# Kernel optimization log

Hardware: AMD Instinct MI355X
Metric: run time of the kernel (lower is better)

Reference implementation:

```python
import jax, jax.numpy as jnp
import numpy as np

RADIUS = 0.2
NSAMPLE = 32
USE_XYZ = True
NORMALIZE_XYZ = False


def setup_inputs() -> dict:
    key = jax.random.key(0)
    k1, k2, k3 = jax.random.split(key, 3)
    B, N, S, C = 4, 8192, 2048, 64
    xyz = jax.random.uniform(k1, (B, N, 3), dtype=jnp.float32)
    new_xyz = jax.random.uniform(k2, (B, S, 3), dtype=jnp.float32)
    features = jax.random.normal(k3, (B, C, N), dtype=jnp.float32)
    return {"xyz": xyz, "new_xyz": new_xyz, "features": features}


def _ball_query(new_xyz, xyz, radius, nsample):
    # squared distances [B, S, N] via ||q||^2 + ||p||^2 - 2 q.p (no [B,S,N,3] blowup)
    q2 = jnp.sum(new_xyz * new_xyz, axis=-1)  # [B, S]
    p2 = jnp.sum(xyz * xyz, axis=-1)          # [B, N]
    qp = jnp.einsum('bsd,bnd->bsn', new_xyz, xyz)
    d2 = q2[:, :, None] + p2[:, None, :] - 2.0 * qp
    N = xyz.shape[1]
    in_ball = d2 < radius * radius
    # CUDA ball_query semantics: first nsample indices (in original point order)
    # inside the ball; unfilled slots replicate the first found index.
    scores = jnp.where(in_ball, jnp.arange(N, dtype=jnp.int32), jnp.int32(N))
    sorted_idx = -jax.lax.top_k(-scores, nsample)[0]  # ascending smallest scores
    first = sorted_idx[..., :1]
    idx = jnp.where(sorted_idx < N, sorted_idx, first)
    idx = jnp.where(first < N, idx, 0)  # no neighbors at all -> index 0
    return idx  # [B, S, nsample] int32


def _group(features, idx):
    # features [B, C, N], idx [B, S, K] -> [B, C, S, K]
    return jax.vmap(lambda f, i: f[:, i])(features, idx)


def reference(xyz, new_xyz, features):
    idx = _ball_query(new_xyz, xyz, RADIUS, NSAMPLE)
    xyz_t = jnp.transpose(xyz, (0, 2, 1))  # [B, 3, N]
    grouped_xyz = _group(xyz_t, idx)  # [B, 3, S, K]
    grouped_xyz = grouped_xyz - jnp.transpose(new_xyz, (0, 2, 1))[..., None]
    if NORMALIZE_XYZ:
        grouped_xyz = grouped_xyz / RADIUS
    grouped_features = _group(features, idx)  # [B, C, S, K]
    if USE_XYZ:
        return jnp.concatenate([grouped_xyz, grouped_features], axis=1)
    return grouped_features
```

## Files before the change

kernel.cpp:

```cpp
#include <hip/hip_runtime.h>
#include <hip/hip_bf16.h>
#include <stdint.h>

#define BB 4
#define NN 8192
#define SS 2048
#define CC 64
#define NS 32

typedef unsigned short ushort8 __attribute__((ext_vector_type(8)));

__device__ __forceinline__ unsigned short f2bf(float f) {
    union { float ff; unsigned int i; } v; v.ff = f;
    unsigned int x = v.i;
    x += 0x7fffu + ((x >> 16) & 1u);
    return (unsigned short)(x >> 16);
}
__device__ __forceinline__ float bf2f(unsigned short u) {
    union { unsigned int i; float f; } v; v.i = ((unsigned int)u) << 16; return v.f;
}

__global__ void stage(const float* __restrict__ xyz,
                      const float* __restrict__ feat,
                      float4* __restrict__ pts,
                      unsigned short* __restrict__ ft) {
#pragma clang fp contract(off)
    const int t = threadIdx.x;
    if (blockIdx.x < 128) {
        int i = blockIdx.x * 256 + t;
        const float* p = xyz + (size_t)i * 3;
        float x = p[0], y = p[1], z = p[2];
        float p2 = x * x;
        p2 += y * y;
        p2 += z * z;
        pts[i] = make_float4(x, y, z, p2);
        return;
    }
    __shared__ float tile[64][65];
    const int blk = blockIdx.x - 128;
    const int b  = blk >> 7;
    const int n0 = (blk & 127) * 64;
    const float* fb = feat + (size_t)b * CC * NN;
    const int nq = t & 15;
    #pragma unroll
    for (int it = 0; it < 4; ++it) {
        int c = it * 16 + (t >> 4);
        float4 v = *(const float4*)(fb + (size_t)c * NN + n0 + nq * 4);
        tile[c][nq * 4 + 0] = v.x;
        tile[c][nq * 4 + 1] = v.y;
        tile[c][nq * 4 + 2] = v.z;
        tile[c][nq * 4 + 3] = v.w;
    }
    __syncthreads();
    unsigned short* fo = ft + ((size_t)b * NN + n0) * CC;
    const int oc = t & 7;
    #pragma unroll
    for (int it = 0; it < 2; ++it) {
        int n = it * 32 + (t >> 3);
        ushort8 w;
        #pragma unroll
        for (int j = 0; j < 8; ++j)
            w[j] = f2bf(tile[oc * 8 + j][n]);
        *(ushort8*)(fo + (size_t)n * CC + oc * 8) = w;
    }
}

__launch_bounds__(256)
__global__ void bq_group(const float* __restrict__ new_xyz,
                         const float4* __restrict__ pts,
                         const unsigned short* __restrict__ ft,
                         float* __restrict__ out) {
#pragma clang fp contract(off)
    __shared__ unsigned long long wmask[2][4];
    __shared__ int sidx[NS];
    __shared__ float sfeat[NS][67];
    const int t    = threadIdx.x;
    const int wave = t >> 6;
    const int lane = t & 63;
    const int blk  = blockIdx.x;
    const int b    = blk >> 11;
    const int s    = blk & (SS - 1);

    const float* q = new_xyz + (size_t)(b * SS + s) * 3;
    const float qx = q[0], qy = q[1], qz = q[2];
    const float4* pb = pts + (size_t)b * NN;

    float q2 = qx * qx;
    q2 += qy * qy;
    q2 += qz * qz;

    const unsigned long long below = (1ull << lane) - 1ull;
    int have = 0;
    float4 p = pb[t];
    #pragma unroll 1
    for (int base = 0; base < NN; base += 256) {
        float4 pn = pb[(base + 256 < NN) ? (base + 256 + t) : t];
        float qp = qx * p.x;
        qp += qy * p.y;
        qp += qz * p.z;
        float t1 = q2 + p.w;
        float d2 = t1 - 2.0f * qp;
        bool in = d2 < 0.04f;
        unsigned long long m = __ballot(in);
        const int buf = (base >> 8) & 1;
        if (lane == 0) wmask[buf][wave] = m;
        __syncthreads();
        unsigned long long m0 = wmask[buf][0], m1 = wmask[buf][1],
                           m2 = wmask[buf][2], m3 = wmask[buf][3];
        int pre = __popcll(m & below);
        if (wave > 0) pre += __popcll(m0);
        if (wave > 1) pre += __popcll(m1);
        if (wave > 2) pre += __popcll(m2);
        int pos = have + pre;
        if (in && pos < NS) sidx[pos] = base + t;
        have += __popcll(m0) + __popcll(m1) + __popcll(m2) + __popcll(m3);
        if (have >= NS) break;
        p = pn;
    }
    __syncthreads();
    if (have < NS) {
        int first = (have == 0) ? 0 : sidx[0];
        if (t < NS && t >= have)
            sidx[t] = (have == 0) ? 0 : first;
    }
    __syncthreads();

    const int k  = t & 31;
    const int oc = t >> 5;
    const int idxk = sidx[k];
    {
        const unsigned short* fr = ft + ((size_t)b * NN + idxk) * CC + oc * 8;
        ushort8 v = *(const ushort8*)fr;
        #pragma unroll
        for (int j = 0; j < 8; ++j)
            sfeat[k][3 + oc * 8 + j] = bf2f(v[j]);
    }
    if (t < 96) {
        const int c = t >> 5;
        float4 p3 = pb[idxk];
        float pc = (c == 0) ? p3.x : (c == 1 ? p3.y : p3.z);
        float qc = (c == 0) ? qx : (c == 1 ? qy : qz);
        sfeat[k][c] = pc - qc;
    }
    __syncthreads();

    const size_t plane = (size_t)SS * NS;
    const size_t ob    = (size_t)b * 67 * plane;
    #pragma unroll
    for (int it = 0; it < 3; ++it) {
        int id = t + it * 256;
        if (id < 67 * 8) {
            int ch = id >> 3;
            int kq = id & 7;
            float4 val = make_float4(sfeat[kq * 4 + 0][ch],
                                     sfeat[kq * 4 + 1][ch],
                                     sfeat[kq * 4 + 2][ch],
                                     sfeat[kq * 4 + 3][ch]);
            *(float4*)(out + ob + (size_t)ch * plane + (size_t)s * NS + kq * 4) = val;
        }
    }
}

extern "C" void kernel_launch(void* const* d_in, const int* in_sizes, int n_in,
                              void* d_out, int out_size, void* d_ws, size_t ws_size,
                              hipStream_t stream) {
    const float* xyz     = (const float*)d_in[0];
    const float* new_xyz = (const float*)d_in[1];
    const float* feat    = (const float*)d_in[2];
    for (int i = 0; i < n_in && i < 3; ++i) {
        if (in_sizes[i] == BB * NN * 3)      xyz     = (const float*)d_in[i];
        else if (in_sizes[i] == BB * SS * 3) new_xyz = (const float*)d_in[i];
        else if (in_sizes[i] == BB * CC * NN) feat   = (const float*)d_in[i];
    }
    float* out = (float*)d_out;

    char* ws = (char*)d_ws;
    float4* pts        = (float4*)ws;
    unsigned short* ft = (unsigned short*)(ws + (size_t)BB * NN * sizeof(float4));

    stage<<<640, 256, 0, stream>>>(xyz, feat, pts, ft);
    bq_group<<<BB * SS, 256, 0, stream>>>(new_xyz, pts, ft, out);
}
```

Baseline: 101.4 us.

## Assign two queries per wave and batch eight queries per block

Changes the ball-query from one query per 256-thread block, which needed block-wide syncs per 256-point chunk, to each wave scanning points independently for two queries with wave-level ballots and no block syncs. A block now handles eight queries and loops over them for the gather and write phase, reusing shared buffers. This removes per-iteration __syncthreads and shares point loads across two queries. The cost is that each wave scans in 64-point steps, so early termination is finer-grained but the scan is more serial per query. The block count also drops eightfold, which may reduce parallelism.

```diff
diff --git a/kernel.cpp b/kernel.cpp
--- a/kernel.cpp
+++ b/kernel.cpp
@@ -7,6 +7,7 @@
 #define SS 2048
 #define CC 64
 #define NS 32
+#define QB 8
 
 typedef unsigned short ushort8 __attribute__((ext_vector_type(8)));
 
@@ -71,93 +72,110 @@
                          const unsigned short* __restrict__ ft,
                          float* __restrict__ out) {
 #pragma clang fp contract(off)
-    __shared__ unsigned long long wmask[2][4];
-    __shared__ int sidx[NS];
+    __shared__ int sidx[QB][NS];
     __shared__ float sfeat[NS][67];
     const int t    = threadIdx.x;
     const int wave = t >> 6;
     const int lane = t & 63;
     const int blk  = blockIdx.x;
-    const int b    = blk >> 11;
-    const int s    = blk & (SS - 1);
-
-    const float* q = new_xyz + (size_t)(b * SS + s) * 3;
-    const float qx = q[0], qy = q[1], qz = q[2];
+    const int b    = blk >> 8;
+    const int s0   = (blk & 255) * QB;
+
     const float4* pb = pts + (size_t)b * NN;
 
-    float q2 = qx * qx;
-    q2 += qy * qy;
-    q2 += qz * qz;
-
-    const unsigned long long below = (1ull << lane) - 1ull;
-    int have = 0;
-    float4 p = pb[t];
-    #pragma unroll 1
-    for (int base = 0; base < NN; base += 256) {
-        float4 pn = pb[(base + 256 < NN) ? (base + 256 + t) : t];
-        float qp = qx * p.x;
-        qp += qy * p.y;
-        qp += qz * p.z;
-        float t1 = q2 + p.w;
-        float d2 = t1 - 2.0f * qp;
-        bool in = d2 < 0.04f;
-        unsigned long long m = __ballot(in);
-        const int buf = (base >> 8) & 1;
-        if (lane == 0) wmask[buf][wave] = m;
-        __syncthreads();
-        unsigned long long m0 = wmask[buf][0], m1 = wmask[buf][1],
-                           m2 = wmask[buf][2], m3 = wmask[buf][3];
-        int pre = __popcll(m & below);
-        if (wave > 0) pre += __popcll(m0);
-        if (wave > 1) pre += __popcll(m1);
-        if (wave > 2) pre += __popcll(m2);
-        int pos = have + pre;
-        if (in && pos < NS) sidx[pos] = base + t;
-        have += __popcll(m0) + __popcll(m1) + __popcll(m2) + __popcll(m3);
-        if (have >= NS) break;
-        p = pn;
+    {
+        const int j0 = 2 * wave;
+        const float* qa = new_xyz + (size_t)(b * SS + s0 + j0) * 3;
+        const float qx0 = qa[0], qy0 = qa[1], qz0 = qa[2];
+        const float qx1 = qa[3], qy1 = qa[4], qz1 = qa[5];
+        float q20 = qx0 * qx0;  q20 += qy0 * qy0;  q20 += qz0 * qz0;
+        float q21 = qx1 * qx1;  q21 += qy1 * qy1;  q21 += qz1 * qz1;
+
+        const unsigned long long below = (1ull << lane) - 1ull;
+        int have0 = 0, have1 = 0, first0 = 0, first1 = 0;
+        float4 p = pb[lane];
+        #pragma unroll 1
+        for (int base = 0; base < NN; base += 64) {
+            const int nb = base + 64;
+            float4 pn = pb[(nb < NN) ? (nb + lane) : lane];
+            if (have0 < NS) {
+                float qp = qx0 * p.x;
+                qp += qy0 * p.y;
+                qp += qz0 * p.z;
+                float t1 = q20 + p.w;
+                float d2 = t1 - 2.0f * qp;
+                bool in = d2 < 0.04f;
+                unsigned long long m = __ballot(in);
+                if (have0 == 0 && m) first0 = base + (int)__builtin_ctzll(m);
+                if (in) {
+                    int pos = have0 + __popcll(m & below);
+                    if (pos < NS) sidx[j0][pos] = base + lane;
+                }
+                have0 += __popcll(m);
+            }
+            if (have1 < NS) {
+                float qp = qx1 * p.x;
+                qp += qy1 * p.y;
+                qp += qz1 * p.z;
+                float t1 = q21 + p.w;
+                float d2 = t1 - 2.0f * qp;
+                bool in = d2 < 0.04f;
+                unsigned long long m = __ballot(in);
+                if (have1 == 0 && m) first1 = base + (int)__builtin_ctzll(m);
+                if (in) {
+                    int pos = have1 + __popcll(m & below);
+                    if (pos < NS) sidx[j0 + 1][pos] = base + lane;
+                }
+                have1 += __popcll(m);
+            }
+            if (have0 >= NS && have1 >= NS) break;
+            p = pn;
+        }
+        if (lane < NS) {
+            if (lane >= have0) sidx[j0][lane]     = (have0 == 0) ? 0 : first0;
+            if (lane >= have1) sidx[j0 + 1][lane] = (have1 == 0) ? 0 : first1;
+        }
     }
     __syncthreads();
-    if (have < NS) {
-        int first = (have == 0) ? 0 : sidx[0];
-        if (t < NS && t >= have)
-            sidx[t] = (have == 0) ? 0 : first;
-    }
-    __syncthreads();
-
+
+    const size_t plane = (size_t)SS * NS;
+    const size_t ob    = (size_t)b * 67 * plane;
     const int k  = t & 31;
     const int oc = t >> 5;
-    const int idxk = sidx[k];
-    {
-        const unsigned short* fr = ft + ((size_t)b * NN + idxk) * CC + oc * 8;
-        ushort8 v = *(const ushort8*)fr;
+    #pragma unroll 1
+    for (int j = 0; j < QB; ++j) {
+        const int s = s0 + j;
+        const int idxk = sidx[j][k];
+        {
+            const unsigned short* fr = ft + ((size_t)b * NN + idxk) * CC + oc * 8;
+            ushort8 v = *(const ushort8*)fr;
+            #pragma unroll
+            for (int jj = 0; jj < 8; ++jj)
+                sfeat[k][3 + oc * 8 + jj] = bf2f(v[jj]);
+        }
+        if (t < 96) {
+            const int c = t >> 5;
+            float4 p3 = pb[idxk];
+            float pc = (c == 0) ? p3.x : (c == 1 ? p3.y : p3.z);
+            float qc = new_xyz[(size_t)(b * SS + s) * 3 + c];
+            sfeat[k][c] = pc - qc;
+        }
+        __syncthreads();
         #pragma unroll
-        for (int j = 0; j < 8; ++j)
-            sfeat[k][3 + oc * 8 + j] = bf2f(v[j]);
-    }
-    if (t < 96) {
-        const int c = t >> 5;
-        float4 p3 = pb[idxk];
-        float pc = (c == 0) ? p3.x : (c == 1 ? p3.y : p3.z);
-        float qc = (c == 0) ? qx : (c == 1 ? qy : qz);
-        sfeat[k][c] = pc - qc;
-    }
-    __syncthreads();
-
-    const size_t plane = (size_t)SS * NS;
-    const size_t ob    = (size_t)b * 67 * plane;
-    #pragma unroll
-    for (int it = 0; it < 3; ++it) {
-        int id = t + it * 256;
-        if (id < 67 * 8) {
-            int ch = id >> 3;
-            int kq = id & 7;
-            float4 val = make_float4(sfeat[kq * 4 + 0][ch],
-                                     sfeat[kq * 4 + 1][ch],
-                                     sfeat[kq * 4 + 2][ch],
-                                     sfeat[kq * 4 + 3][ch]);
-            *(float4*)(out + ob + (size_t)ch * plane + (size_t)s * NS + kq * 4) = val;
-        }
+        for (int it = 0; it < 3; ++it) {
+            int id = t + it * 256;
+            if (id < 67 * 8) {
+                int ch = id >> 3;
+                int kq = id & 7;
+                float4 val = make_float4(sfeat[kq * 4 + 0][ch],
+                                         sfeat[kq * 4 + 1][ch],
+                                         sfeat[kq * 4 + 2][ch],
+                                         sfeat[kq * 4 + 3][ch]);
+                *(float4*)(out + ob + (size_t)ch * plane +
+                           (size_t)s * NS + kq * 4) = val;
+            }
+        }
+        __syncthreads();
     }
 }
 
@@ -179,5 +197,5 @@
     unsigned short* ft = (unsigned short*)(ws + (size_t)BB * NN * sizeof(float4));
 
     stage<<<640, 256, 0, stream>>>(xyz, feat, pts, ft);
-    bq_group<<<BB * SS, 256, 0, stream>>>(new_xyz, pts, ft, out);
-}
+    bq_group<<<BB * SS / QB, 256, 0, stream>>>(new_xyz, pts, ft, out);
+}
```

Result: slower. 114.7 us (+13.1%).
